# Kernel tuning notes

Hardware: AMD Instinct MI355X
Metric: run time of the kernel (lower is better)

The kernel has to match this reference:

```python
import jax, jax.numpy as jnp
import numpy as np

N = 100000
E = 3200000


def setup_inputs() -> dict:
    key = jax.random.key(0)
    k1, k2, k3 = jax.random.split(key, 3)
    x = jax.random.normal(k1, (N, 256), dtype=jnp.float32)
    edge_index = jax.random.randint(k2, (2, E), 0, N, dtype=jnp.int64)
    W = jax.random.normal(k3, (256, 64), dtype=jnp.float32) * (1.0 / np.sqrt(256.0))
    b = jnp.zeros((64,), dtype=jnp.float32)
    return {"x": x, "edge_index": edge_index, "W": W, "b": b}


def reference(x, edge_index, W, b):
    # GCNConv (PyG defaults): add self-loops, symmetric deg normalization,
    # linear transform, neighbor aggregation, bias.
    n = x.shape[0]
    loops = jnp.arange(n, dtype=edge_index.dtype)
    row = jnp.concatenate([edge_index[0], loops])  # src
    col = jnp.concatenate([edge_index[1], loops])  # dst

    # degree over destination nodes (incl. self-loops)
    deg = jax.ops.segment_sum(jnp.ones_like(col, dtype=x.dtype), col, num_segments=n)
    deg_inv_sqrt = jnp.where(deg > 0, jax.lax.rsqrt(deg), 0.0)
    norm = deg_inv_sqrt[row] * deg_inv_sqrt[col]  # [E+N]

    h = x @ W  # [N, C]
    msgs = h[row] * norm[:, None]  # gather + scale
    out = jax.ops.segment_sum(msgs, col, num_segments=n)  # scatter-add
    return out + b
```

## Files before the change

### kernel.cpp

```cpp
#include <hip/hip_runtime.h>

#define C_IN 256
#define C_OUT 64
#define BSH 7
#define NPB 128
#define NB 1024
#define CHUNK 8192
#define RG 32
#define SCAP 6144

typedef short bf16x8 __attribute__((ext_vector_type(8)));
typedef float f32x4 __attribute__((ext_vector_type(4)));

__device__ __forceinline__ unsigned short f2bf(float f) {
    unsigned u = __builtin_bit_cast(unsigned, f);
    u = (u + 0x7FFFu + ((u >> 16) & 1u)) >> 16;
    return (unsigned short)u;
}
__device__ __forceinline__ float bflo(unsigned u) {
    return __builtin_bit_cast(float, u << 16);
}
__device__ __forceinline__ float bfhi(unsigned u) {
    return __builtin_bit_cast(float, u & 0xffff0000u);
}

__global__ __launch_bounds__(256) void k_wt(const float* __restrict__ W,
                                            unsigned short* __restrict__ WTs) {
#pragma unroll
    for (int i = 0; i < 16; ++i) {
        int f = i * 256 + threadIdx.x;
        int k = f >> 4;
        int n4 = (f & 15) * 4;
        float4 v = ((const float4*)W)[f];
        int c = k >> 3, ci = k & 7;
        float vv[4] = {v.x, v.y, v.z, v.w};
#pragma unroll
        for (int r = 0; r < 4; ++r) {
            int row = n4 + r;
            WTs[row * 256 + ((c ^ (row & 7)) << 3) + ci] = f2bf(vv[r]);
        }
    }
}

__global__ __launch_bounds__(1024) void k_hist2(const int* __restrict__ dst,
                                                int* __restrict__ table, int e) {
    __shared__ int cnt[NB];
    cnt[threadIdx.x] = 0;
    __syncthreads();
    int b0 = blockIdx.x * CHUNK;
#pragma unroll
    for (int k = 0; k < CHUNK / 1024; ++k) {
        int i = b0 + k * 1024 + threadIdx.x;
        if (i < e) atomicAdd(&cnt[dst[i] >> BSH], 1);
    }
    __syncthreads();
    table[(size_t)blockIdx.x * NB + threadIdx.x] = cnt[threadIdx.x];
}

__global__ __launch_bounds__(256) void kA2(int* __restrict__ table,
                                           int* __restrict__ tot, int nbin) {
    __shared__ int part[256];
    int t = threadIdx.x;
    int bc = t & 15, rg = t >> 4;
    int B = blockIdx.x * 16 + bc;
    int v[RG];
    int s = 0;
#pragma unroll
    for (int i = 0; i < RG; ++i) {
        int r = rg * RG + i;
        int x = (r < nbin) ? table[(size_t)r * NB + B] : 0;
        v[i] = s;
        s += x;
    }
    part[t] = s;
    __syncthreads();
#pragma unroll
    for (int off = 1; off < 16; off <<= 1) {
        int u = (rg >= off) ? part[t - off * 16] : 0;
        __syncthreads();
        part[t] += u;
        __syncthreads();
    }
    int incl = part[t];
    int base = incl - s;
#pragma unroll
    for (int i = 0; i < RG; ++i) {
        int r = rg * RG + i;
        if (r < nbin) table[(size_t)r * NB + B] = base + v[i];
    }
    if (rg == 15) tot[B] = incl;
}

__global__ __launch_bounds__(1024) void kB(const int* __restrict__ tot,
                                           int* __restrict__ gbase, int e) {
    __shared__ int l[NB];
    int t = threadIdx.x;
    int v = tot[t];
    l[t] = v;
    __syncthreads();
    for (int off = 1; off < NB; off <<= 1) {
        int u = (t >= off) ? l[t - off] : 0;
        __syncthreads();
        l[t] += u;
        __syncthreads();
    }
    gbase[t] = l[t] - v;
    if (t == NB - 1) gbase[NB] = e;
}

__global__ __launch_bounds__(1024) void k_bin2(const int* __restrict__ src,
                                               const int* __restrict__ dst,
                                               const int* __restrict__ table,
                                               const int* __restrict__ gbase,
                                               int* __restrict__ sorted, int e) {
    __shared__ int stage[CHUNK];
    __shared__ unsigned short sbkt[CHUNK];
    __shared__ int lcnt[NB];
    __shared__ int lsc[NB];
    __shared__ int lbase[NB];
    int t = threadIdx.x;
    lcnt[t] = 0;
    __syncthreads();
    int b0 = blockIdx.x * CHUNK;

    int bb[CHUNK / 1024], pv[CHUNK / 1024], rk[CHUNK / 1024];
#pragma unroll
    for (int k = 0; k < CHUNK / 1024; ++k) {
        int i = b0 + k * 1024 + t;
        if (i < e) {
            int d = dst[i];
            bb[k] = d >> BSH;
            pv[k] = (src[i] << BSH) | (d & (NPB - 1));
            rk[k] = atomicAdd(&lcnt[bb[k]], 1);
        } else {
            bb[k] = -1;
        }
    }
    __syncthreads();
    lsc[t] = lcnt[t];
    __syncthreads();
    for (int off = 1; off < NB; off <<= 1) {
        int u = (t >= off) ? lsc[t - off] : 0;
        __syncthreads();
        lsc[t] += u;
        __syncthreads();
    }
    lbase[t] = lsc[t] - lcnt[t];
    __syncthreads();
    int tot = lsc[NB - 1];

#pragma unroll
    for (int k = 0; k < CHUNK / 1024; ++k) {
        if (bb[k] >= 0) {
            int p = lbase[bb[k]] + rk[k];
            stage[p] = pv[k];
            sbkt[p] = (unsigned short)bb[k];
        }
    }
    lcnt[t] = gbase[t] + table[(size_t)blockIdx.x * NB + t];
    __syncthreads();

#pragma unroll
    for (int k = 0; k < CHUNK / 1024; ++k) {
        int j = k * 1024 + t;
        if (j < tot) {
            int B = sbkt[j];
            sorted[lcnt[B] + (j - lbase[B])] = stage[j];
        }
    }
}

__global__ __launch_bounds__(512) void k_sort2(const int* __restrict__ sorted,
                                               const int* __restrict__ gbase,
                                               int* __restrict__ eidx,
                                               int* __restrict__ rowptr,
                                               float* __restrict__ dinv, int n, int e) {
    __shared__ int cnt[NPB];
    __shared__ int sc[NPB];
    __shared__ int cur[NPB];
    __shared__ int sstage[SCAP];
    int b = blockIdx.x;
    int node0 = b * NPB;
    int range = min(NPB, n - node0);
    int inbase = gbase[b];
    int m_b = gbase[b + 1] - inbase;
    bool fits = (m_b <= SCAP);
    if (threadIdx.x < NPB) cnt[threadIdx.x] = 0;
    if (fits)
        for (int j = threadIdx.x; j < m_b; j += 512) sstage[j] = sorted[inbase + j];
    __syncthreads();
    for (int j = threadIdx.x; j < m_b; j += 512) {
        int v = fits ? sstage[j] : sorted[inbase + j];
        atomicAdd(&cnt[v & (NPB - 1)], 1);
    }
    __syncthreads();
    if (threadIdx.x < NPB) sc[threadIdx.x] = cnt[threadIdx.x];
    __syncthreads();
    for (int off = 1; off < NPB; off <<= 1) {
        int t = (threadIdx.x < NPB && threadIdx.x >= off) ? sc[threadIdx.x - off] : 0;
        __syncthreads();
        if (threadIdx.x < NPB) sc[threadIdx.x] += t;
        __syncthreads();
    }
    if (threadIdx.x < NPB) {
        int excl = inbase + sc[threadIdx.x] - cnt[threadIdx.x];
        cur[threadIdx.x] = excl;
        if (threadIdx.x < range) {
            rowptr[node0 + threadIdx.x] = excl;
            dinv[node0 + threadIdx.x] = rsqrtf((float)(cnt[threadIdx.x] + 1));
        }
    }
    __syncthreads();
    for (int j = threadIdx.x; j < m_b; j += 512) {
        int v = fits ? sstage[j] : sorted[inbase + j];
        int pos = atomicAdd(&cur[v & (NPB - 1)], 1);
        eidx[pos] = v >> BSH;
    }
    if (b == 0 && threadIdx.x == 0) rowptr[n] = e;
}

__global__ __launch_bounds__(256, 3) void k_gemm(const float* __restrict__ x,
                                                 const unsigned short* __restrict__ WTs,
                                                 const float* __restrict__ dinv,
                                                 unsigned short* __restrict__ h, int n) {
    __shared__ unsigned short Wl[64 * 256];

    const int t = threadIdx.x;
    const int lane = t & 63;
    const int wv = t >> 6;
    const int m = lane & 15;
    const int q = lane >> 4;
    const int mx = m & 7;

    if (blockIdx.x == 0 && t < 8)
        *(uint4*)&h[(size_t)n * C_OUT + t * 8] = make_uint4(0u, 0u, 0u, 0u);

#pragma unroll
    for (int j = 0; j < 8; ++j) {
        const unsigned short* gsrc = WTs + j * 2048 + wv * 512 + lane * 8;
        unsigned short* ldst = Wl + j * 2048 + wv * 512;
        __builtin_amdgcn_global_load_lds(
            (const __attribute__((address_space(1))) unsigned int*)gsrc,
            (__attribute__((address_space(3))) unsigned int*)ldst, 16, 0, 0);
    }

    int arow = blockIdx.x * 64 + 16 * wv + m;
    const float* xp = x + (size_t)(arow < n ? arow : 0) * C_IN + q * 8;
    float4 raw[16];
#pragma unroll
    for (int ks = 0; ks < 8; ++ks) {
        const float* p0 = xp + ks * 32;
        const float* p1 = xp + ks * 32 + 4;
        asm volatile("global_load_dwordx4 %0, %1, off" : "=v"(raw[2 * ks]) : "v"(p0));
        asm volatile("global_load_dwordx4 %0, %1, off" : "=v"(raw[2 * ks + 1]) : "v"(p1));
    }

    asm volatile("s_waitcnt vmcnt(0)" ::: "memory");
    __builtin_amdgcn_sched_barrier(0);
    __syncthreads();

    float di[4];
#pragma unroll
    for (int r = 0; r < 4; ++r) {
        int gr = blockIdx.x * 64 + 16 * wv + q * 4 + r;
        di[r] = dinv[gr < n ? gr : 0];
    }

    bf16x8 A[8];
#pragma unroll
    for (int ks = 0; ks < 8; ++ks) {
        float4 v0 = raw[2 * ks];
        float4 v1 = raw[2 * ks + 1];
        bf16x8 a;
        a[0] = (short)f2bf(v0.x); a[1] = (short)f2bf(v0.y);
        a[2] = (short)f2bf(v0.z); a[3] = (short)f2bf(v0.w);
        a[4] = (short)f2bf(v1.x); a[5] = (short)f2bf(v1.y);
        a[6] = (short)f2bf(v1.z); a[7] = (short)f2bf(v1.w);
        A[ks] = a;
    }

    f32x4 acc[4];
#pragma unroll
    for (int nt = 0; nt < 4; ++nt) acc[nt] = (f32x4){0.f, 0.f, 0.f, 0.f};

#pragma unroll
    for (int ks = 0; ks < 8; ++ks) {
        int c = ks * 4 + q;
        int cs = (c ^ mx) << 3;
#pragma unroll
        for (int nt = 0; nt < 4; ++nt) {
            bf16x8 B = *(const bf16x8*)&Wl[(nt * 16 + m) * 256 + cs];
            acc[nt] = __builtin_amdgcn_mfma_f32_16x16x32_bf16(A[ks], B, acc[nt], 0, 0, 0);
        }
    }

#pragma unroll
    for (int r = 0; r < 4; ++r) {
        int gr = blockIdx.x * 64 + 16 * wv + q * 4 + r;
        if (gr < n) {
#pragma unroll
            for (int nt = 0; nt < 4; ++nt)
                h[(size_t)gr * C_OUT + nt * 16 + m] = f2bf(acc[nt][r] * di[r]);
        }
    }
}

#define GROUND(T, HV)                                                                   \
    {                                                                                   \
        int s_ = __shfl(eid, (T) * 8 + g, 64);                                          \
        const unsigned short* p_ = h + (size_t)s_ * C_OUT + c8;                         \
        asm volatile("global_load_dwordx4 %0, %1, off" : "=v"(HV) : "v"(p_));           \
    }
#define ACC8(HV)                                                                        \
    {                                                                                   \
        a0 += bflo(HV.x); a1 += bfhi(HV.x); a2 += bflo(HV.y); a3 += bfhi(HV.y);         \
        a4 += bflo(HV.z); a5 += bfhi(HV.z); a6 += bflo(HV.w); a7 += bfhi(HV.w);         \
    }

__global__ __launch_bounds__(256) void k_gather(const int* __restrict__ rowptr,
                                                const int* __restrict__ eidx,
                                                const unsigned short* __restrict__ h,
                                                const float* __restrict__ dinv,
                                                const float* __restrict__ bias,
                                                float* __restrict__ out, int n) {
    int node = blockIdx.x * 4 + (threadIdx.x >> 6);
    if (node >= n) return;
    int lane = threadIdx.x & 63;
    int g = lane >> 3;
    int c8 = (lane & 7) * 8;

    int beg = rowptr[node];
    int end = rowptr[node + 1];
    int cnt = end - beg;

    float a0 = 0.f, a1 = 0.f, a2 = 0.f, a3 = 0.f;
    float a4 = 0.f, a5 = 0.f, a6 = 0.f, a7 = 0.f;

    {
        int idx = beg + lane;
        int eid = (idx < end) ? eidx[idx] : n;
        uint4 hv0, hv1, hv2, hv3, hv4, hv5, hv6, hv7;
        GROUND(0, hv0); GROUND(1, hv1); GROUND(2, hv2); GROUND(3, hv3);
        bool more = cnt > 32;
        if (more) { GROUND(4, hv4); GROUND(5, hv5); GROUND(6, hv6); GROUND(7, hv7); }
        asm volatile("s_waitcnt vmcnt(0)" ::: "memory");
        __builtin_amdgcn_sched_barrier(0);
        ACC8(hv0); ACC8(hv1); ACC8(hv2); ACC8(hv3);
        if (more) { ACC8(hv4); ACC8(hv5); ACC8(hv6); ACC8(hv7); }
    }
    for (int j = beg + 64; j < end; j += 64) {
        int idx = j + lane;
        int eid = (idx < end) ? eidx[idx] : n;
        uint4 hv0, hv1, hv2, hv3, hv4, hv5, hv6, hv7;
        GROUND(0, hv0); GROUND(1, hv1); GROUND(2, hv2); GROUND(3, hv3);
        bool more = (end - j) > 32;
        if (more) { GROUND(4, hv4); GROUND(5, hv5); GROUND(6, hv6); GROUND(7, hv7); }
        asm volatile("s_waitcnt vmcnt(0)" ::: "memory");
        __builtin_amdgcn_sched_barrier(0);
        ACC8(hv0); ACC8(hv1); ACC8(hv2); ACC8(hv3);
        if (more) { ACC8(hv4); ACC8(hv5); ACC8(hv6); ACC8(hv7); }
    }

#pragma unroll
    for (int off = 8; off < 64; off <<= 1) {
        a0 += __shfl_xor(a0, off, 64); a1 += __shfl_xor(a1, off, 64);
        a2 += __shfl_xor(a2, off, 64); a3 += __shfl_xor(a3, off, 64);
        a4 += __shfl_xor(a4, off, 64); a5 += __shfl_xor(a5, off, 64);
        a6 += __shfl_xor(a6, off, 64); a7 += __shfl_xor(a7, off, 64);
    }
    if (g == 0) {
        float di = dinv[node];
        uint4 sv = *(const uint4*)&h[(size_t)node * C_OUT + c8];
        float4 b0 = *(const float4*)&bias[c8];
        float4 b1 = *(const float4*)&bias[c8 + 4];
        float4 o0, o1;
        o0.x = (a0 + bflo(sv.x)) * di + b0.x;
        o0.y = (a1 + bfhi(sv.x)) * di + b0.y;
        o0.z = (a2 + bflo(sv.y)) * di + b0.z;
        o0.w = (a3 + bfhi(sv.y)) * di + b0.w;
        o1.x = (a4 + bflo(sv.z)) * di + b1.x;
        o1.y = (a5 + bfhi(sv.z)) * di + b1.y;
        o1.z = (a6 + bflo(sv.w)) * di + b1.z;
        o1.w = (a7 + bfhi(sv.w)) * di + b1.w;
        *(float4*)&out[(size_t)node * C_OUT + c8] = o0;
        *(float4*)&out[(size_t)node * C_OUT + c8 + 4] = o1;
    }
}

extern "C" void kernel_launch(void* const* d_in, const int* in_sizes, int n_in,
                              void* d_out, int out_size, void* d_ws, size_t ws_size,
                              hipStream_t stream) {
    const float* x = (const float*)d_in[0];
    const int* ei = (const int*)d_in[1];
    const float* W = (const float*)d_in[2];
    const float* bias = (const float*)d_in[3];
    float* out = (float*)d_out;

    const int n = in_sizes[0] / C_IN;
    const int e = in_sizes[1] / 2;
    const int* src = ei;
    const int* dst = ei + e;

    const int nbin = (e + CHUNK - 1) / CHUNK;
    const int nbuck = (n + NPB - 1) / NPB;

    char* w = (char*)d_ws;
    unsigned short* h = (unsigned short*)w;  w += ((size_t)n + 1) * C_OUT * 2;
    int* sorted = (int*)w;                   w += (size_t)e * 4;
    int* eidx = (int*)w;                     w += (size_t)e * 4;
    float* dinv = (float*)w;                 w += (size_t)n * 4;
    int* rowptr = (int*)w;                   w += (size_t)(n + 1) * 4;
    int* table = (int*)w;                    w += (size_t)nbin * NB * 4;
    int* tot = (int*)w;                      w += NB * 4;
    int* gbase = (int*)w;                    w += (NB + 1) * 4;
    unsigned short* WTs = (unsigned short*)w; w += (size_t)C_OUT * C_IN * 2;

    k_wt<<<1, 256, 0, stream>>>(W, WTs);
    k_hist2<<<nbin, 1024, 0, stream>>>(dst, table, e);
    kA2<<<NB / 16, 256, 0, stream>>>(table, tot, nbin);
    kB<<<1, 1024, 0, stream>>>(tot, gbase, e);
    k_bin2<<<nbin, 1024, 0, stream>>>(src, dst, table, gbase, sorted, e);
    k_sort2<<<nbuck, 512, 0, stream>>>(sorted, gbase, eidx, rowptr, dinv, n, e);
    k_gemm<<<(n + 63) / 64, 256, 0, stream>>>(x, WTs, dinv, h, n);
    k_gather<<<(n + 3) / 4, 256, 0, stream>>>(rowptr, eidx, h, dinv, bias, out, n);
}
```

Before: 287.2 us.

## Process two 64-row tiles per GEMM block with overlapped x loads

Each k_gemm block now handles 128 rows as two 64-row halves. It issues the second half's x loads before computing the first half, so the W-to-LDS staging is amortised over twice the rows and memory latency overlaps with MFMA work. The full __syncthreads is replaced by a partial vmcnt wait plus s_barrier, and dinv is read in the epilogue. This raises register pressure from the extra 16 float4 buffers and halves the grid size, which may reduce occupancy and latency hiding.

```diff
diff --git a/kernel.cpp b/kernel.cpp
--- a/kernel.cpp
+++ b/kernel.cpp
@@ -219,6 +219,20 @@
     if (b == 0 && threadIdx.x == 0) rowptr[n] = e;
 }
 
+#define LDX2(R0, R1, P, O1, O2)                                                          \
+    asm volatile("global_load_dwordx4 %0, %1, off offset:" #O1 : "=v"(R0) : "v"(P));     \
+    asm volatile("global_load_dwordx4 %0, %1, off offset:" #O2 : "=v"(R1) : "v"(P));
+
+#define LDBATCH(RAW, P)                                                                  \
+    LDX2(RAW[0], RAW[1], P, 0, 16)                                                       \
+    LDX2(RAW[2], RAW[3], P, 128, 144)                                                    \
+    LDX2(RAW[4], RAW[5], P, 256, 272)                                                    \
+    LDX2(RAW[6], RAW[7], P, 384, 400)                                                    \
+    LDX2(RAW[8], RAW[9], P, 512, 528)                                                    \
+    LDX2(RAW[10], RAW[11], P, 640, 656)                                                  \
+    LDX2(RAW[12], RAW[13], P, 768, 784)                                                  \
+    LDX2(RAW[14], RAW[15], P, 896, 912)
+
 __global__ __launch_bounds__(256, 3) void k_gemm(const float* __restrict__ x,
                                                  const unsigned short* __restrict__ WTs,
                                                  const float* __restrict__ dinv,
@@ -235,6 +249,14 @@
     if (blockIdx.x == 0 && t < 8)
         *(uint4*)&h[(size_t)n * C_OUT + t * 8] = make_uint4(0u, 0u, 0u, 0u);
 
+    int rowA = blockIdx.x * 128 + 16 * wv + m;
+    int rowB = rowA + 64;
+    const float* xpA = x + (size_t)(rowA < n ? rowA : 0) * C_IN + q * 8;
+    const float* xpB = x + (size_t)(rowB < n ? rowB : 0) * C_IN + q * 8;
+
+    float4 rawA[16];
+    LDBATCH(rawA, xpA)
+    __builtin_amdgcn_sched_barrier(0);
 #pragma unroll
     for (int j = 0; j < 8; ++j) {
         const unsigned short* gsrc = WTs + j * 2048 + wv * 512 + lane * 8;
@@ -243,34 +265,19 @@
             (const __attribute__((address_space(1))) unsigned int*)gsrc,
             (__attribute__((address_space(3))) unsigned int*)ldst, 16, 0, 0);
     }
-
-    int arow = blockIdx.x * 64 + 16 * wv + m;
-    const float* xp = x + (size_t)(arow < n ? arow : 0) * C_IN + q * 8;
-    float4 raw[16];
+    __builtin_amdgcn_sched_barrier(0);
+    float4 rawB[16];
+    LDBATCH(rawB, xpB)
+    __builtin_amdgcn_sched_barrier(0);
+
+    asm volatile("s_waitcnt vmcnt(16)" ::: "memory");
+    __builtin_amdgcn_sched_barrier(0);
+
+    bf16x8 A[8];
 #pragma unroll
     for (int ks = 0; ks < 8; ++ks) {
-        const float* p0 = xp + ks * 32;
-        const float* p1 = xp + ks * 32 + 4;
-        asm volatile("global_load_dwordx4 %0, %1, off" : "=v"(raw[2 * ks]) : "v"(p0));
-        asm volatile("global_load_dwordx4 %0, %1, off" : "=v"(raw[2 * ks + 1]) : "v"(p1));
-    }
-
-    asm volatile("s_waitcnt vmcnt(0)" ::: "memory");
-    __builtin_amdgcn_sched_barrier(0);
-    __syncthreads();
-
-    float di[4];
-#pragma unroll
-    for (int r = 0; r < 4; ++r) {
-        int gr = blockIdx.x * 64 + 16 * wv + q * 4 + r;
-        di[r] = dinv[gr < n ? gr : 0];
-    }
-
-    bf16x8 A[8];
-#pragma unroll
-    for (int ks = 0; ks < 8; ++ks) {
-        float4 v0 = raw[2 * ks];
-        float4 v1 = raw[2 * ks + 1];
+        float4 v0 = rawA[2 * ks];
+        float4 v1 = rawA[2 * ks + 1];
         bf16x8 a;
         a[0] = (short)f2bf(v0.x); a[1] = (short)f2bf(v0.y);
         a[2] = (short)f2bf(v0.z); a[3] = (short)f2bf(v0.w);
@@ -279,14 +286,14 @@
         A[ks] = a;
     }
 
+    __builtin_amdgcn_s_barrier();
+
     f32x4 acc[4];
 #pragma unroll
     for (int nt = 0; nt < 4; ++nt) acc[nt] = (f32x4){0.f, 0.f, 0.f, 0.f};
-
 #pragma unroll
     for (int ks = 0; ks < 8; ++ks) {
-        int c = ks * 4 + q;
-        int cs = (c ^ mx) << 3;
+        int cs = ((ks * 4 + q) ^ mx) << 3;
 #pragma unroll
         for (int nt = 0; nt < 4; ++nt) {
             bf16x8 B = *(const bf16x8*)&Wl[(nt * 16 + m) * 256 + cs];
@@ -294,13 +301,51 @@
         }
     }
 
+    asm volatile("s_waitcnt vmcnt(0)" ::: "memory");
+    __builtin_amdgcn_sched_barrier(0);
+
 #pragma unroll
     for (int r = 0; r < 4; ++r) {
-        int gr = blockIdx.x * 64 + 16 * wv + q * 4 + r;
+        int gr = blockIdx.x * 128 + 16 * wv + q * 4 + r;
         if (gr < n) {
+            float di = dinv[gr];
 #pragma unroll
             for (int nt = 0; nt < 4; ++nt)
-                h[(size_t)gr * C_OUT + nt * 16 + m] = f2bf(acc[nt][r] * di[r]);
+                h[(size_t)gr * C_OUT + nt * 16 + m] = f2bf(acc[nt][r] * di);
+        }
+    }
+
+    bf16x8 Bf[8];
+#pragma unroll
+    for (int ks = 0; ks < 8; ++ks) {
+        float4 v0 = rawB[2 * ks];
+        float4 v1 = rawB[2 * ks + 1];
+        bf16x8 a;
+        a[0] = (short)f2bf(v0.x); a[1] = (short)f2bf(v0.y);
+        a[2] = (short)f2bf(v0.z); a[3] = (short)f2bf(v0.w);
+        a[4] = (short)f2bf(v1.x); a[5] = (short)f2bf(v1.y);
+        a[6] = (short)f2bf(v1.z); a[7] = (short)f2bf(v1.w);
+        Bf[ks] = a;
+    }
+#pragma unroll
+    for (int nt = 0; nt < 4; ++nt) acc[nt] = (f32x4){0.f, 0.f, 0.f, 0.f};
+#pragma unroll
+    for (int ks = 0; ks < 8; ++ks) {
+        int cs = ((ks * 4 + q) ^ mx) << 3;
+#pragma unroll
+        for (int nt = 0; nt < 4; ++nt) {
+            bf16x8 B = *(const bf16x8*)&Wl[(nt * 16 + m) * 256 + cs];
+            acc[nt] = __builtin_amdgcn_mfma_f32_16x16x32_bf16(Bf[ks], B, acc[nt], 0, 0, 0);
+        }
+    }
+#pragma unroll
+    for (int r = 0; r < 4; ++r) {
+        int gr = blockIdx.x * 128 + 64 + 16 * wv + q * 4 + r;
+        if (gr < n) {
+            float di = dinv[gr];
+#pragma unroll
+            for (int nt = 0; nt < 4; ++nt)
+                h[(size_t)gr * C_OUT + nt * 16 + m] = f2bf(acc[nt][r] * di);
         }
     }
 }
@@ -421,6 +466,6 @@
     kB<<<1, 1024, 0, stream>>>(tot, gbase, e);
     k_bin2<<<nbin, 1024, 0, stream>>>(src, dst, table, gbase, sorted, e);
     k_sort2<<<nbuck, 512, 0, stream>>>(sorted, gbase, eidx, rowptr, dinv, n, e);
-    k_gemm<<<(n + 63) / 64, 256, 0, stream>>>(x, WTs, dinv, h, n);
+    k_gemm<<<(n + 127) / 128, 256, 0, stream>>>(x, WTs, dinv, h, n);
     k_gather<<<(n + 3) / 4, 256, 0, stream>>>(rowptr, eidx, h, dinv, bias, out, n);
 }
```

Result: no change. 289.6 us (+0.9%).
